# Optimization experiments

Hardware: AMD Instinct MI355X
Metric: run time of the kernel (lower is better)

Reference implementation:

```python
import jax, jax.numpy as jnp
import numpy as np

K = 121          # kernel_size
C = 3            # channels
PAD = (K - 1) // 2  # 60, replicate padding so output matches input spatial size


def setup_inputs() -> dict:
    key = jax.random.key(0)
    k1, k2 = jax.random.split(key)
    x = jax.random.normal(k1, (8, C, 512, 512), dtype=jnp.float32)
    sigma = jax.random.uniform(k2, (), dtype=jnp.float32)
    return {"x": x, "sigma": sigma}


def _gaussian_kernel(sigma):
    # sigma -> sigma*8 + 16, variance = sigma**2 (as in torch forward)
    s = sigma * 8.0 + 16.0
    variance = s * s
    coord = jnp.arange(K, dtype=jnp.float32) - (K - 1) / 2.0  # centered coords
    diff = -(coord[:, None] ** 2 + coord[None, :] ** 2)       # [K,K], -((x-m)^2+(y-m)^2)
    kern = jnp.exp(diff / (2.0 * variance))
    # the 1/(2*pi*variance) prefactor cancels under normalization
    kern = kern / jnp.sum(kern)
    return kern


def reference(x, sigma):
    kern = _gaussian_kernel(sigma)
    # depthwise weights: [out_ch=C, in_ch/groups=1, K, K]
    w = jnp.broadcast_to(kern[None, None, :, :], (C, 1, K, K))
    # replicate padding (torch 'replicate' == jnp 'edge')
    xp = jnp.pad(x, ((0, 0), (0, 0), (PAD, PAD), (PAD, PAD)), mode="edge")
    out = jax.lax.conv_general_dilated(
        xp, w,
        window_strides=(1, 1),
        padding="VALID",
        dimension_numbers=("NCHW", "OIHW", "NCHW"),
        feature_group_count=C,
    )
    return out
```

## Files before the change

### kernel.cpp

```cpp
#include <hip/hip_runtime.h>


#define HH    512
#define WW    512
#define PLANE (512 * 512)
#define NIMG  24
#define ROWF  672

__global__ void wk_prep(const float* __restrict__ sigma,
                        float* __restrict__ wg) {
    const int tid = threadIdx.x;
    const float s = sigma[0] * 8.0f + 16.0f;
    const float inv2v = 1.0f / (2.0f * s * s);
    float sum = 0.0f;
    #pragma unroll
    for (int k = 0; k <= 120; ++k) {
        const float c = (float)k - 60.0f;
        sum += __expf(-c * c * inv2v);
    }
    float g = 0.0f;
    if (tid < 121) {
        const float c = (float)tid - 60.0f;
        g = __expf(-c * c * inv2v);
    }
    wg[tid] = g / sum;
}

__device__ __forceinline__ int swz_off(int col) {
    const int u = col >> 2;
    return ((u ^ ((u >> 3) & 7)) << 2) + (col & 3);
}

#define V_OCT(CUR, NXT, KO)                                               \
    { *(float4*)&wq[0] = *(const float4*)&wg[(KO) * 8];                   \
      *(float4*)&wq[4] = *(const float4*)&wg[(KO) * 8 + 4];               \
      _Pragma("unroll")                                                   \
      for (int ki = 0; ki < 8; ++ki) {                                    \
          int rr = r0 - 52 + (KO) * 8 + ki;                               \
          rr = rr < 0 ? 0 : (rr > HH - 1 ? HH - 1 : rr);                  \
          NXT[ki] = *(const float2*)&src[(size_t)rr * WW];                \
          const float wk = wq[ki];                                        \
          _Pragma("unroll")                                               \
          for (int j = 0; j < 8; ++j) {                                   \
              const int idx = ki + j;                                     \
              const float2 v = (idx < 8) ? CUR[idx] : NXT[idx - 8];       \
              vac[j].x += wk * v.x; vac[j].y += wk * v.y;                 \
          }                                                               \
      }                                                                   \
    }

#define LOADG2(DA, DB, G)                                                 \
    { const int u_  = 2 * (G);                                            \
      const int o1_ = (u_ ^ ((u_ >> 3) & 7)) << 2;                        \
      const int o2_ = o1_ ^ 4;                                            \
      *(float4*)&DA[0] = *(const float4*)(bs + o1_);                      \
      *(float4*)&DA[4] = *(const float4*)(bs + o2_);                      \
      *(float4*)&DB[0] = *(const float4*)(bs + o1_ + 256);                \
      *(float4*)&DB[4] = *(const float4*)(bs + o2_ + 256); }

#define H_OCT2(A0, A1, A2, A3, B0, B1, B2, B3, KO)                        \
    { LOADG2(A3, B3, L + (KO) + 3)                                        \
      *(float4*)&wq[0] = *(const float4*)&wg[(KO) * 8];                   \
      *(float4*)&wq[4] = *(const float4*)&wg[(KO) * 8 + 4];               \
      _Pragma("unroll")                                                   \
      for (int ki = 0; ki < 8; ++ki) {                                    \
          const float wk = wq[ki];                                        \
          _Pragma("unroll")                                               \
          for (int j = 0; j < 8; ++j) {                                   \
              const int idx = ki + j;                                     \
              const float vA = (idx < 8) ? A0[idx]                        \
                             : (idx < 16) ? A1[idx - 8] : A2[idx - 16];   \
              const float vB = (idx < 8) ? B0[idx]                        \
                             : (idx < 16) ? B1[idx - 8] : B2[idx - 16];   \
              accA[j] += wk * vA;                                         \
              accB[j] += wk * vB;                                         \
          }                                                               \
      }                                                                   \
    }

__global__ __launch_bounds__(256, 6) void blur_fused(
        const float* __restrict__ x, const float* __restrict__ wg,
        float* __restrict__ out) {
    __shared__ float sm[8 * ROWF];
    const int tid = threadIdx.x;

    const int lid   = blockIdx.x + gridDim.x * blockIdx.y;
    const int tile  = (lid & 7) * 192 + (lid >> 3);
    const int r0    = (tile & 63) * 8;
    const int plane = tile >> 6;

    const int c0 = tid * 2;
    const float* __restrict__ src = x + (size_t)plane * PLANE + c0;

    float2 wa[8], wb[8], vac[8];
    float  wq[8];
    #pragma unroll
    for (int m = 0; m < 8; ++m) {
        int rr = r0 - 60 + m;
        rr = rr < 0 ? 0 : rr;
        wa[m] = *(const float2*)&src[(size_t)rr * WW];
    }
    #pragma unroll
    for (int j = 0; j < 8; ++j) vac[j] = make_float2(0.f, 0.f);

    #pragma unroll 1
    for (int ko = 0; ko < 16; ko += 2) {
        V_OCT(wa, wb, ko)
        V_OCT(wb, wa, ko + 1)
    }

    {
        const int off = swz_off(c0 + 60);
        #pragma unroll
        for (int j = 0; j < 8; ++j)
            *(float2*)&sm[j * ROWF + off] = vac[j];
    }
    __syncthreads();

    if (tid < 36) {
        const int p = (tid < 15) ? tid * 4
                    : (tid < 34) ? 572 + (tid - 15) * 4
                                 : 648 + (tid - 34) * 4;
        const int u   = p >> 2;
        const int off = (u ^ ((u >> 3) & 7)) << 2;
        const int soff = (tid < 15) ? swz_off(60) : swz_off(571);
        #pragma unroll
        for (int r8 = 0; r8 < 8; ++r8) {
            const float v = (tid < 34) ? sm[r8 * ROWF + soff] : 0.0f;
            *(float4*)&sm[r8 * ROWF + off] = make_float4(v, v, v, v);
        }
    }
    __syncthreads();

    const int r = tid >> 5;
    const int L = tid & 31;
    const float* __restrict__ bs = sm + r * ROWF;

    float a0[8], a1[8], a2[8], a3[8];
    float b0[8], b1[8], b2[8], b3[8];
    float accA[8], accB[8];
    #pragma unroll
    for (int j = 0; j < 8; ++j) { accA[j] = 0.0f; accB[j] = 0.0f; }

    LOADG2(a0, b0, L)
    LOADG2(a1, b1, L + 1)
    LOADG2(a2, b2, L + 2)

    #pragma unroll 1
    for (int ko = 0; ko < 16; ko += 4) {
        H_OCT2(a0, a1, a2, a3, b0, b1, b2, b3, ko)
        H_OCT2(a1, a2, a3, a0, b1, b2, b3, b0, ko + 1)
        H_OCT2(a2, a3, a0, a1, b2, b3, b0, b1, ko + 2)
        H_OCT2(a3, a0, a1, a2, b3, b0, b1, b2, ko + 3)
    }

    float* __restrict__ dst = out + (size_t)plane * PLANE
                                  + (size_t)(r0 + r) * WW + L * 8;
    *(float4*)(dst)       = make_float4(accA[0], accA[1], accA[2], accA[3]);
    *(float4*)(dst + 4)   = make_float4(accA[4], accA[5], accA[6], accA[7]);
    *(float4*)(dst + 256) = make_float4(accB[0], accB[1], accB[2], accB[3]);
    *(float4*)(dst + 260) = make_float4(accB[4], accB[5], accB[6], accB[7]);
}

extern "C" void kernel_launch(void* const* d_in, const int* in_sizes, int n_in,
                              void* d_out, int out_size, void* d_ws, size_t ws_size,
                              hipStream_t stream) {
    const float* x     = (const float*)d_in[0];
    const float* sigma = (const float*)d_in[1];
    float* out = (float*)d_out;
    float* wg  = (float*)d_ws;
    wk_prep<<<dim3(1), dim3(128), 0, stream>>>(sigma, wg);
    blur_fused<<<dim3(HH / 8, NIMG), dim3(256), 0, stream>>>(x, wg, out);
}
```

Measured before the change: 116.2 us.

## Double row tile height to sixteen rows per block in separable blur

Each block now computes 16 output rows instead of 8. The vertical pass keeps three rotating 8-row register windows and 16 float2 accumulators, and the horizontal pass loops twice over the shared tile. This spreads the vertical halo loads (120 extra rows per tile) over more output rows, so fewer redundant global reads are issued per output. In exchange, register pressure rises, the launch bound drops to 3 blocks per CU, the grid is halved, and the shared-memory tile doubles in size.

```diff
diff --git a/kernel.cpp b/kernel.cpp
--- a/kernel.cpp
+++ b/kernel.cpp
@@ -5,6 +5,7 @@
 #define WW    512
 #define PLANE (512 * 512)
 #define NIMG  24
+#define TH    16
 #define ROWF  672
 
 __global__ void wk_prep(const float* __restrict__ sigma,
@@ -31,19 +32,20 @@
     return ((u ^ ((u >> 3) & 7)) << 2) + (col & 3);
 }
 
-#define V_OCT(CUR, NXT, KO)                                               \
+#define V_OCT3(C0, C1, NXT, KO)                                           \
     { *(float4*)&wq[0] = *(const float4*)&wg[(KO) * 8];                   \
       *(float4*)&wq[4] = *(const float4*)&wg[(KO) * 8 + 4];               \
       _Pragma("unroll")                                                   \
       for (int ki = 0; ki < 8; ++ki) {                                    \
-          int rr = r0 - 52 + (KO) * 8 + ki;                               \
+          int rr = r0 - 44 + (KO) * 8 + ki;                               \
           rr = rr < 0 ? 0 : (rr > HH - 1 ? HH - 1 : rr);                  \
           NXT[ki] = *(const float2*)&src[(size_t)rr * WW];                \
           const float wk = wq[ki];                                        \
           _Pragma("unroll")                                               \
-          for (int j = 0; j < 8; ++j) {                                   \
+          for (int j = 0; j < 16; ++j) {                                  \
               const int idx = ki + j;                                     \
-              const float2 v = (idx < 8) ? CUR[idx] : NXT[idx - 8];       \
+              const float2 v = (idx < 8) ? C0[idx]                        \
+                             : (idx < 16) ? C1[idx - 8] : NXT[idx - 16];  \
               vac[j].x += wk * v.x; vac[j].y += wk * v.y;                 \
           }                                                               \
       }                                                                   \
@@ -78,41 +80,49 @@
       }                                                                   \
     }
 
-__global__ __launch_bounds__(256, 6) void blur_fused(
+__global__ __launch_bounds__(256, 3) void blur_fused(
         const float* __restrict__ x, const float* __restrict__ wg,
         float* __restrict__ out) {
-    __shared__ float sm[8 * ROWF];
+    __shared__ float sm[TH * ROWF];
     const int tid = threadIdx.x;
 
     const int lid   = blockIdx.x + gridDim.x * blockIdx.y;
-    const int tile  = (lid & 7) * 192 + (lid >> 3);
-    const int r0    = (tile & 63) * 8;
-    const int plane = tile >> 6;
+    const int tile  = (lid & 7) * 96 + (lid >> 3);
+    const int r0    = (tile & 31) * TH;
+    const int plane = tile >> 5;
 
     const int c0 = tid * 2;
     const float* __restrict__ src = x + (size_t)plane * PLANE + c0;
 
-    float2 wa[8], wb[8], vac[8];
+    float2 w0[8], w1[8], w2[8], vac[16];
     float  wq[8];
     #pragma unroll
     for (int m = 0; m < 8; ++m) {
         int rr = r0 - 60 + m;
         rr = rr < 0 ? 0 : rr;
-        wa[m] = *(const float2*)&src[(size_t)rr * WW];
+        w0[m] = *(const float2*)&src[(size_t)rr * WW];
     }
     #pragma unroll
-    for (int j = 0; j < 8; ++j) vac[j] = make_float2(0.f, 0.f);
+    for (int m = 0; m < 8; ++m) {
+        int rr = r0 - 52 + m;
+        rr = rr < 0 ? 0 : rr;
+        w1[m] = *(const float2*)&src[(size_t)rr * WW];
+    }
+    #pragma unroll
+    for (int j = 0; j < 16; ++j) vac[j] = make_float2(0.f, 0.f);
 
     #pragma unroll 1
-    for (int ko = 0; ko < 16; ko += 2) {
-        V_OCT(wa, wb, ko)
-        V_OCT(wb, wa, ko + 1)
+    for (int ko = 0; ko < 15; ko += 3) {
+        V_OCT3(w0, w1, w2, ko)
+        V_OCT3(w1, w2, w0, ko + 1)
+        V_OCT3(w2, w0, w1, ko + 2)
     }
+    V_OCT3(w0, w1, w2, 15)
 
     {
         const int off = swz_off(c0 + 60);
         #pragma unroll
-        for (int j = 0; j < 8; ++j)
+        for (int j = 0; j < TH; ++j)
             *(float2*)&sm[j * ROWF + off] = vac[j];
     }
     __syncthreads();
@@ -125,7 +135,7 @@
         const int off = (u ^ ((u >> 3) & 7)) << 2;
         const int soff = (tid < 15) ? swz_off(60) : swz_off(571);
         #pragma unroll
-        for (int r8 = 0; r8 < 8; ++r8) {
+        for (int r8 = 0; r8 < TH; ++r8) {
             const float v = (tid < 34) ? sm[r8 * ROWF + soff] : 0.0f;
             *(float4*)&sm[r8 * ROWF + off] = make_float4(v, v, v, v);
         }
@@ -134,32 +144,37 @@
 
     const int r = tid >> 5;
     const int L = tid & 31;
-    const float* __restrict__ bs = sm + r * ROWF;
-
-    float a0[8], a1[8], a2[8], a3[8];
-    float b0[8], b1[8], b2[8], b3[8];
-    float accA[8], accB[8];
-    #pragma unroll
-    for (int j = 0; j < 8; ++j) { accA[j] = 0.0f; accB[j] = 0.0f; }
-
-    LOADG2(a0, b0, L)
-    LOADG2(a1, b1, L + 1)
-    LOADG2(a2, b2, L + 2)
 
     #pragma unroll 1
-    for (int ko = 0; ko < 16; ko += 4) {
-        H_OCT2(a0, a1, a2, a3, b0, b1, b2, b3, ko)
-        H_OCT2(a1, a2, a3, a0, b1, b2, b3, b0, ko + 1)
-        H_OCT2(a2, a3, a0, a1, b2, b3, b0, b1, ko + 2)
-        H_OCT2(a3, a0, a1, a2, b3, b0, b1, b2, ko + 3)
+    for (int pass = 0; pass < 2; ++pass) {
+        const float* __restrict__ bs = sm + (r + 8 * pass) * ROWF;
+
+        float a0[8], a1[8], a2[8], a3[8];
+        float b0[8], b1[8], b2[8], b3[8];
+        float accA[8], accB[8];
+        #pragma unroll
+        for (int j = 0; j < 8; ++j) { accA[j] = 0.0f; accB[j] = 0.0f; }
+
+        LOADG2(a0, b0, L)
+        LOADG2(a1, b1, L + 1)
+        LOADG2(a2, b2, L + 2)
+
+        #pragma unroll 1
+        for (int ko = 0; ko < 16; ko += 4) {
+            H_OCT2(a0, a1, a2, a3, b0, b1, b2, b3, ko)
+            H_OCT2(a1, a2, a3, a0, b1, b2, b3, b0, ko + 1)
+            H_OCT2(a2, a3, a0, a1, b2, b3, b0, b1, ko + 2)
+            H_OCT2(a3, a0, a1, a2, b3, b0, b1, b2, ko + 3)
+        }
+
+        float* __restrict__ dst = out + (size_t)plane * PLANE
+                                      + (size_t)(r0 + r + 8 * pass) * WW
+                                      + L * 8;
+        *(float4*)(dst)       = make_float4(accA[0], accA[1], accA[2], accA[3]);
+        *(float4*)(dst + 4)   = make_float4(accA[4], accA[5], accA[6], accA[7]);
+        *(float4*)(dst + 256) = make_float4(accB[0], accB[1], accB[2], accB[3]);
+        *(float4*)(dst + 260) = make_float4(accB[4], accB[5], accB[6], accB[7]);
     }
-
-    float* __restrict__ dst = out + (size_t)plane * PLANE
-                                  + (size_t)(r0 + r) * WW + L * 8;
-    *(float4*)(dst)       = make_float4(accA[0], accA[1], accA[2], accA[3]);
-    *(float4*)(dst + 4)   = make_float4(accA[4], accA[5], accA[6], accA[7]);
-    *(float4*)(dst + 256) = make_float4(accB[0], accB[1], accB[2], accB[3]);
-    *(float4*)(dst + 260) = make_float4(accB[4], accB[5], accB[6], accB[7]);
 }
 
 extern "C" void kernel_launch(void* const* d_in, const int* in_sizes, int n_in,
@@ -170,5 +185,5 @@
     float* out = (float*)d_out;
     float* wg  = (float*)d_ws;
     wk_prep<<<dim3(1), dim3(128), 0, stream>>>(sigma, wg);
-    blur_fused<<<dim3(HH / 8, NIMG), dim3(256), 0, stream>>>(x, wg, out);
+    blur_fused<<<dim3(HH / TH, NIMG), dim3(256), 0, stream>>>(x, wg, out);
 }
```

New measurement: 142.7 us. +22.8%, slower.
